# Kernel optimization log

Measured on AMD Instinct MI355X. Metric: run time of the kernel, lower is better.

The kernel has to match this reference:

```python
import jax, jax.numpy as jnp
import numpy as np
import math

B, T, C = 2, 2048, 1024
H, D = 16, 64
GAMMA = 8

def setup_inputs() -> dict:
    key = jax.random.key(0)
    ks = jax.random.split(key, 6)
    s = 1.0 / math.sqrt(C)  # keep pre-softmax scores well-scaled
    return {
        "x": jax.random.normal(ks[0], (B, T, C), jnp.float32),
        "Wq": jax.random.normal(ks[1], (C, 2 * C), jnp.float32) * s,
        "Wk": jax.random.normal(ks[2], (C, 2 * C), jnp.float32) * s,
        "Wv": jax.random.normal(ks[3], (C, C), jnp.float32) * s,
        "Wo": jax.random.normal(ks[4], (C, C), jnp.float32) * s,
        "theta_offset": jax.random.normal(ks[5], (H,), jnp.float32) * 0.1,
    }

def _heads(t):  # (B,T,C) -> (B,H,T,D)
    return t.reshape(B, T, H, D).transpose(0, 2, 1, 3)

def reference(x, Wq, Wk, Wv, Wo, theta_offset):
    scale = 1.0 / math.sqrt(D)
    q_raw = x @ Wq            # (B,T,2C)
    k_raw = x @ Wk
    v = _heads(x @ Wv)        # (B,H,T,D)
    q_amp, q_phase = _heads(q_raw[..., :C]), _heads(q_raw[..., C:])
    k_amp, k_phase = _heads(k_raw[..., :C]), _heads(k_raw[..., C:])
    q_amp = jax.nn.softplus(q_amp)
    k_amp = jax.nn.softplus(k_amp)
    # sum_d a_q a_k cos(p_q - p_k) = (a_q cos p_q)(a_k cos p_k) + (a_q sin p_q)(a_k sin p_k)
    qc, qs = q_amp * jnp.cos(q_phase), q_amp * jnp.sin(q_phase)
    kc, ks_ = k_amp * jnp.cos(k_phase), k_amp * jnp.sin(k_phase)
    scores = (jnp.einsum('bhqd,bhkd->bhqk', qc, kc)
              + jnp.einsum('bhqd,bhkd->bhqk', qs, ks_)) * scale
    if T > GAMMA:  # theta gating
        cid = jnp.arange(T, dtype=jnp.float32) / GAMMA
        cycle_dist = cid[None, :] - cid[:, None]          # (T,T): cid[j]-cid[i]
        gate = jnp.cos(theta_offset[:, None, None] * cycle_dist[None])  # (H,T,T)
        scores = scores * gate[None]
    causal = jnp.tril(jnp.ones((T, T), dtype=bool))
    scores = jnp.where(causal[None, None], scores, -jnp.inf)
    attn = jax.nn.softmax(scores, axis=-1)
    out = jnp.einsum('bhqk,bhkd->bhqd', attn, v)
    out = out.transpose(0, 2, 1, 3).reshape(B, T, C)
    return out @ Wo
```

## Files before the change

### kernel.cpp

```cpp
#include <hip/hip_runtime.h>
#include <cmath>

namespace {

constexpr int B_ = 2, T_ = 2048, C_ = 1024, H_ = 16;
constexpr float GAMMA_INV = 0.125f;
constexpr float SCALE = 0.125f;
constexpr float LOG2E = 1.4426950408889634f;
constexpr float THR2 = 11.5415603f;

typedef __attribute__((ext_vector_type(8))) short bf16x8;
typedef __attribute__((ext_vector_type(4))) float f32x4;
typedef unsigned short ushort_t;

__device__ __forceinline__ ushort_t f2bf(float x) {
  union { float f; unsigned int u; } v; v.f = x;
  unsigned int r = (v.u + 0x7fffu + ((v.u >> 16) & 1u)) >> 16;
  return (ushort_t)r;
}

__device__ __forceinline__ unsigned pk_bf16(float a, float b) {
  unsigned r;
  asm("v_cvt_pk_bf16_f32 %0, %1, %2" : "=v"(r) : "v"(a), "v"(b));
  return r;
}

__device__ __forceinline__ float fexp2(float x) {
  return __builtin_amdgcn_exp2f(x);
}

__device__ __forceinline__ f32x4 mfma16(bf16x8 a, bf16x8 b, f32x4 c) {
  return __builtin_amdgcn_mfma_f32_16x16x32_bf16(a, b, c, 0, 0, 0);
}

__device__ __forceinline__ void gld_lds16(const ushort_t* g, ushort_t* l) {
  __builtin_amdgcn_global_load_lds(
      (const __attribute__((address_space(1))) unsigned int*)g,
      (__attribute__((address_space(3))) unsigned int*)l, 16, 0, 0);
}

constexpr int GBM = 128, GBN = 128, GBK = 64;

#define GEMM_CORE(A_, Bt_, K_)                                                  \
  __shared__ ushort_t As[GBM][GBK];                                             \
  __shared__ ushort_t Bs[GBN][GBK];                                             \
  const int tid = threadIdx.x;                                                  \
  const int wv = tid >> 6;                                                      \
  const int ln = tid & 63;                                                      \
  const int lr = ln & 15, hi = ln >> 4;                                         \
  const int wr = wv >> 1, wc = wv & 1;                                          \
  const int srow8 = tid >> 3;                            \
  const int ssw = ((tid & 7) ^ (srow8 & 7)) * 8;       \
  const int kxg = (lr & 7) << 3;                    \
  f32x4 acc[4][4];                                                              \
  _Pragma("unroll")                                                             \
  for (int m = 0; m < 4; ++m)                                                   \
    _Pragma("unroll")                                                           \
    for (int n = 0; n < 4; ++n)                                                 \
      _Pragma("unroll")                                                         \
      for (int r = 0; r < 4; ++r) acc[m][n][r] = 0.0f;                          \
  for (int k0 = 0; k0 < K_; k0 += GBK) {                                        \
    _Pragma("unroll")                                                           \
    for (int p = 0; p < 4; ++p) {                                               \
      gld_lds16(A_ + (size_t)(m0 + p * 32 + srow8) * K_ + k0 + ssw,             \
                &As[0][0] + p * 2048 + wv * 512);                               \
      gld_lds16(Bt_ + (size_t)(n0 + p * 32 + srow8) * K_ + k0 + ssw,            \
                &Bs[0][0] + p * 2048 + wv * 512);                               \
    }                                                                           \
    __syncthreads();                                                            \
    _Pragma("unroll")                                                           \
    for (int ks = 0; ks < 2; ++ks) {                                            \
      bf16x8 af[4], bfr[4];                                                     \
      _Pragma("unroll")                                                         \
      for (int m = 0; m < 4; ++m)                                               \
        af[m] = *(const bf16x8*)&As[wr * 64 + m * 16 + lr]                      \
                                  [(ks * 32 + hi * 8) ^ kxg];                   \
      _Pragma("unroll")                                                         \
      for (int n = 0; n < 4; ++n)                                               \
        bfr[n] = *(const bf16x8*)&Bs[wc * 64 + n * 16 + lr]                     \
                                   [(ks * 32 + hi * 8) ^ kxg];                  \
      _Pragma("unroll")                                                         \
      for (int m = 0; m < 4; ++m)                                               \
        _Pragma("unroll")                                                       \
        for (int n = 0; n < 4; ++n)                                             \
          acc[m][n] = mfma16(af[m], bfr[n], acc[m][n]);                         \
    }                                                                           \
    __syncthreads();                                                            \
  }

__global__ __launch_bounds__(256) void gemm_f32out(const ushort_t* __restrict__ A,
                                                   const ushort_t* __restrict__ Bt,
                                                   float* __restrict__ Cm,
                                                   int N, int K) {
  const int m0 = blockIdx.y * GBM, n0 = blockIdx.x * GBN;
  GEMM_CORE(A, Bt, K)
  #pragma unroll
  for (int m = 0; m < 4; ++m) {
    #pragma unroll
    for (int r = 0; r < 4; ++r) {
      const int row = m0 + wr * 64 + m * 16 + hi * 4 + r;
      float* Crow = Cm + (size_t)row * N + n0 + wc * 64;
      #pragma unroll
      for (int n = 0; n < 4; ++n)
        Crow[n * 16 + lr] = acc[m][n][r];
    }
  }
}

__global__ __launch_bounds__(256) void gemm_qkv(const ushort_t* __restrict__ A,
                                                const ushort_t* __restrict__ Bt,
                                                ushort_t* __restrict__ Qb,
                                                ushort_t* __restrict__ Kb,
                                                float* __restrict__ Vf,
                                                int K) {
  const int m0 = blockIdx.y * GBM, n0 = blockIdx.x * GBN;
  GEMM_CORE(A, Bt, K)
  if (n0 < 4096) {
    const int isK = (n0 >> 11) & 1;
    ushort_t* Dst = isK ? Kb : Qb;
    const int odd = lr & 1;
    #pragma unroll
    for (int m = 0; m < 4; ++m) {
      #pragma unroll
      for (int r = 0; r < 4; ++r) {
        const int row = m0 + wr * 64 + m * 16 + hi * 4 + r;
        #pragma unroll
        for (int n = 0; n < 4; ++n) {
          const int nn = n0 + wc * 64 + n * 16 + lr;
          float x = acc[m][n][r];
          float y = __shfl_xor(x, 1);
          float amp = odd ? y : x;
          float ph  = odd ? x : y;
          float sp = (amp > 20.f) ? amp : __logf(1.0f + __expf(amp));
          float val = sp * (odd ? __sinf(ph) : __cosf(ph));
          const int cc = (nn & 2047) >> 1;
          const int h = cc >> 6, d = cc & 63;
          const int t = row & (T_ - 1), b = row >> 11;
          Dst[(((size_t)(b * H_ + h) * T_) + t) * 128 + d + (odd ? 64 : 0)] = f2bf(val);
        }
      }
    }
  } else {
    const int v0 = n0 - 4096;
    #pragma unroll
    for (int m = 0; m < 4; ++m) {
      #pragma unroll
      for (int r = 0; r < 4; ++r) {
        const int row = m0 + wr * 64 + m * 16 + hi * 4 + r;
        float* Crow = Vf + (size_t)row * 1024 + v0 + wc * 64;
        #pragma unroll
        for (int n = 0; n < 4; ++n)
          Crow[n * 16 + lr] = acc[m][n][r];
      }
    }
  }
}

__global__ __launch_bounds__(256) void f32_to_bf16(const float* __restrict__ in,
                                                   ushort_t* __restrict__ out) {
  const int i = (blockIdx.x * 256 + threadIdx.x) * 4;
  float4 a = *(const float4*)&in[i];
  uint2 p;
  p.x = (unsigned)f2bf(a.x) | ((unsigned)f2bf(a.y) << 16);
  p.y = (unsigned)f2bf(a.z) | ((unsigned)f2bf(a.w) << 16);
  *(uint2*)&out[i] = p;
}

__global__ __launch_bounds__(256) void wt_bf16(const float* __restrict__ W,
                                               ushort_t* __restrict__ Wt,
                                               int K, int N) {
  __shared__ ushort_t t[32][33];
  const int k0 = blockIdx.y * 32, n0 = blockIdx.x * 32;
  const int i = threadIdx.x;
  const int r = i >> 3, c4 = (i & 7) * 4;
  float4 v = *(const float4*)&W[(size_t)(k0 + r) * N + n0 + c4];
  t[r][c4 + 0] = f2bf(v.x); t[r][c4 + 1] = f2bf(v.y);
  t[r][c4 + 2] = f2bf(v.z); t[r][c4 + 3] = f2bf(v.w);
  __syncthreads();
  ushort_t o0 = t[c4 + 0][r], o1 = t[c4 + 1][r], o2 = t[c4 + 2][r], o3 = t[c4 + 3][r];
  uint2 p;
  p.x = (unsigned)o0 | ((unsigned)o1 << 16);
  p.y = (unsigned)o2 | ((unsigned)o3 << 16);
  *(uint2*)&Wt[(size_t)(n0 + r) * K + k0 + c4] = p;
}

__global__ __launch_bounds__(256) void wt_qk(const float* __restrict__ Wq,
                                             const float* __restrict__ Wk,
                                             ushort_t* __restrict__ Wqkt) {
  __shared__ float t[32][33];
  const int k0 = blockIdx.x * 32, n0 = blockIdx.y * 32;
  const float* src = (n0 < 2048) ? Wq : Wk;
  const int c0 = (n0 & 2047) >> 1;
  const int i = threadIdx.x;
  {
    const int r = i >> 3, c4 = (i & 7) * 4;
    const int scol = (c4 < 16) ? (c0 + c4) : (1024 + c0 + c4 - 16);
    float4 v = *(const float4*)&src[(size_t)(k0 + r) * 2048 + scol];
    t[r][c4 + 0] = v.x; t[r][c4 + 1] = v.y; t[r][c4 + 2] = v.z; t[r][c4 + 3] = v.w;
  }
  __syncthreads();
  {
    const int orow = i >> 3, k4 = (i & 7) * 4;
    const int sel = (orow >> 1) + ((orow & 1) ? 16 : 0);
    uint2 p;
    p.x = (unsigned)f2bf(t[k4 + 0][sel]) | ((unsigned)f2bf(t[k4 + 1][sel]) << 16);
    p.y = (unsigned)f2bf(t[k4 + 2][sel]) | ((unsigned)f2bf(t[k4 + 3][sel]) << 16);
    *(uint2*)&Wqkt[(size_t)(n0 + orow) * 1024 + k0 + k4] = p;
  }
}

__global__ __launch_bounds__(256) void v_transpose(const float* __restrict__ V,
                                                   ushort_t* __restrict__ VT) {
  const int bh = blockIdx.y;
  const int b = bh >> 4, h = bh & 15;
  const int t0 = blockIdx.x * 32;
  __shared__ ushort_t lds[32][72];
  const int i = threadIdx.x;
  {
    int r = i >> 3, d0 = (i & 7) * 8;
    const float* src = V + ((size_t)(b * T_) + t0 + r) * C_ + h * 64 + d0;
    float4 a = *(const float4*)src;
    float4 c = *(const float4*)(src + 4);
    lds[r][d0 + 0] = f2bf(a.x); lds[r][d0 + 1] = f2bf(a.y);
    lds[r][d0 + 2] = f2bf(a.z); lds[r][d0 + 3] = f2bf(a.w);
    lds[r][d0 + 4] = f2bf(c.x); lds[r][d0 + 5] = f2bf(c.y);
    lds[r][d0 + 6] = f2bf(c.z); lds[r][d0 + 7] = f2bf(c.w);
  }
  __syncthreads();
  {
    int d = i >> 2, tq = (i & 3) * 8;
    ushort_t tmp[8];
    #pragma unroll
    for (int j = 0; j < 8; ++j) tmp[j] = lds[tq + j][d];
    ulonglong2 pk;
    pk.x = (unsigned long long)tmp[0] | ((unsigned long long)tmp[1] << 16) |
           ((unsigned long long)tmp[2] << 32) | ((unsigned long long)tmp[3] << 48);
    pk.y = (unsigned long long)tmp[4] | ((unsigned long long)tmp[5] << 16) |
           ((unsigned long long)tmp[6] << 32) | ((unsigned long long)tmp[7] << 48);
    *(ulonglong2*)(VT + ((size_t)bh * 64 + d) * T_ + t0 + tq) = pk;
  }
}

__global__ __launch_bounds__(256) void attn_split(const ushort_t* __restrict__ Q,
                                                  const ushort_t* __restrict__ K,
                                                  const ushort_t* __restrict__ VT,
                                                  const float* __restrict__ theta,
                                                  unsigned* __restrict__ Op,
                                                  float* __restrict__ mpart,
                                                  float* __restrict__ lpart) {
  const int id = blockIdx.x;
  const int xcd = id & 7, sub = id >> 3;
  const int bhl = sub / 40;
  const int u = 39 - (sub - bhl * 40);
  int qt, s, ns;
  if (u < 4)       { qt = u;                 s = 0;             ns = 1; }
  else if (u < 12) { qt = 4 + ((u - 4) >> 1);  s = (u - 4) & 1;   ns = 2; }
  else if (u < 24) { qt = 8 + (u - 12) / 3;    s = (u - 12) % 3;  ns = 3; }
  else             { qt = 12 + ((u - 24) >> 2); s = (u - 24) & 3; ns = 4; }
  const int nktf = 2 * qt + 2;
  const int t0 = (s * nktf) / ns;
  const int t1 = ((s + 1) * nktf) / ns;
  const int bh = xcd * 4 + bhl;
  const int p = bh * 40 + u;
  unsigned* Op_my = Op + (size_t)p * 4096;

  const int h = bh & 15;
  const int tid = threadIdx.x;
  const int wid = tid >> 6, lane = tid & 63;
  const int q_base = qt * 128 + wid * 32;
  const int lr = lane & 15, lg = lane >> 4;
  const int kx = (lr & 7) << 4;

  __shared__ alignas(16) ushort_t Ksh[2][64 * 128];
  __shared__ alignas(16) ushort_t Vsh[64 * 64];

  const float th = theta[h];
  const int q_lo = q_base + lr;
  const int q_hi = q_base + 16 + lr;

  bf16x8 qfl[4], qfh[4];
  {
    const ushort_t* Qrow = Q + ((size_t)bh * T_ + q_lo) * 128 + lg * 8;
    #pragma unroll
    for (int ks = 0; ks < 4; ++ks) {
      qfl[ks] = *(const bf16x8*)(Qrow + ks * 32);
      qfh[ks] = *(const bf16x8*)(Qrow + 16 * 128 + ks * 32);
    }
  }

  const float cql = cosf(th * (float)q_lo * GAMMA_INV) * (SCALE * LOG2E);
  const float sql = sinf(th * (float)q_lo * GAMMA_INV) * (SCALE * LOG2E);
  const float cqh = cosf(th * (float)q_hi * GAMMA_INV) * (SCALE * LOG2E);
  const float sqh = sinf(th * (float)q_hi * GAMMA_INV) * (SCALE * LOG2E);
  float ck[4], sk[4];
  #pragma unroll
  for (int r = 0; r < 4; ++r) {
    float ang = th * (float)(t0 * 64 + lg * 4 + r) * GAMMA_INV;
    ck[r] = cosf(ang); sk[r] = sinf(ang);
  }
  float Ajl[4], Bjl[4], Ajh[4], Bjh[4];
  {
    const float c2 = cosf(th * 2.0f), s2 = sinf(th * 2.0f);
    float cj = 1.0f, sj = 0.0f;
    #pragma unroll
    for (int j = 0; j < 4; ++j) {
      Ajl[j] = cql * cj + sql * sj;
      Bjl[j] = sql * cj - cql * sj;
      Ajh[j] = cqh * cj + sqh * sj;
      Bjh[j] = sqh * cj - cqh * sj;
      float t0r = cj * c2 - sj * s2;
      sj = sj * c2 + cj * s2;
      cj = t0r;
    }
  }
  const float cd8 = cosf(th * 8.0f), sd8 = sinf(th * 8.0f);

  f32x4 o_lo[4], o_hi[4];
  #pragma unroll
  for (int n = 0; n < 4; ++n)
    #pragma unroll
    for (int r = 0; r < 4; ++r) { o_lo[n][r] = 0.0f; o_hi[n][r] = 0.0f; }
  float m_lo = -1e30f, l_lo = 0.0f, m_hi = -1e30f, l_hi = 0.0f;

  const ushort_t* Kbh = K + (size_t)bh * T_ * 128;
  const int srow = lane >> 4;
  const int scol = (lane & 15) * 8;
  const int vd = tid >> 2;
  const int vce = (tid & 3) * 16;
  const ushort_t* Vgb = VT + ((size_t)bh * 64 + vd) * T_ + vce;
  uint4 vreg[2];

  {
    const int k0 = t0 * 64;
    #pragma unroll
    for (int c = 0; c < 4; ++c) {
      const int r7 = 4 * (c & 1) + srow;
      const ushort_t* src = Kbh + (size_t)(k0 + 16 * wid + 4 * c + srow) * 128
                            + (scol ^ (r7 << 3));
      gld_lds16(src, &Ksh[0][(wid * 4 + c) * 512]);
    }
    #pragma unroll
    for (int c = 0; c < 2; ++c) vreg[c] = *(const uint4*)(Vgb + k0 + c * 8);
    #pragma unroll
    for (int c = 0; c < 2; ++c) {
      int byte = (vce * 2 + c * 16) ^ ((vd & 7) << 4);
      *(uint4*)&Vsh[vd * 64 + (byte >> 1)] = vreg[c];
    }
  }
  __syncthreads();

  for (int kt = t0; kt < t1; ++kt) {
    const int cur = (kt - t0) & 1;
    const int k0 = kt * 64;
    const bool more = (kt + 1) < t1;
    if (more) {
      const int kn = (kt + 1) * 64;
      #pragma unroll
      for (int c = 0; c < 4; ++c) {
        const int r7 = 4 * (c & 1) + srow;
        const ushort_t* src = Kbh + (size_t)(kn + 16 * wid + 4 * c + srow) * 128
                              + (scol ^ (r7 << 3));
        gld_lds16(src, &Ksh[cur ^ 1][(wid * 4 + c) * 512]);
      }
      #pragma unroll
      for (int c = 0; c < 2; ++c) vreg[c] = *(const uint4*)(Vgb + kn + c * 8);
    }
    f32x4 sl[4], sh[4];
    #pragma unroll
    for (int j = 0; j < 4; ++j)
      #pragma unroll
      for (int r = 0; r < 4; ++r) { sl[j][r] = 0.0f; sh[j][r] = 0.0f; }
    #pragma unroll
    for (int j = 0; j < 4; ++j) {
      const int rbase = (j * 16 + lr) * 128;
      #pragma unroll
      for (int ks = 0; ks < 4; ++ks) {
        const int byte = (ks * 64 + lg * 16) ^ kx;
        bf16x8 kf = *(const bf16x8*)&Ksh[cur][rbase + (byte >> 1)];
        sl[j] = mfma16(kf, qfl[ks], sl[j]);
        sh[j] = mfma16(kf, qfh[ks], sh[j]);
      }
    }
    float vl[4][4], vh[4][4];
    #pragma unroll
    for (int j = 0; j < 4; ++j)
      #pragma unroll
      for (int r = 0; r < 4; ++r) {
        const int kk = k0 + j * 16 + lg * 4 + r;
        float xl = sl[j][r] * (Ajl[j] * ck[r] + Bjl[j] * sk[r]);
        float xh = sh[j][r] * (Ajh[j] * ck[r] + Bjh[j] * sk[r]);
        vl[j][r] = (kk > q_lo) ? -3e30f : xl;
        vh[j][r] = (kk > q_hi) ? -3e30f : xh;
      }
    float tml = vl[0][0], tmh = vh[0][0];
    #pragma unroll
    for (int j = 0; j < 4; ++j)
      #pragma unroll
      for (int r = 0; r < 4; ++r) { tml = fmaxf(tml, vl[j][r]); tmh = fmaxf(tmh, vh[j][r]); }
    tml = fmaxf(tml, __shfl_xor(tml, 16));
    tml = fmaxf(tml, __shfl_xor(tml, 32));
    tmh = fmaxf(tmh, __shfl_xor(tmh, 16));
    tmh = fmaxf(tmh, __shfl_xor(tmh, 32));
    if (__ballot(tml > m_lo + THR2 || tmh > m_hi + THR2)) {
      float mnl = fmaxf(m_lo, tml), mnh = fmaxf(m_hi, tmh);
      float el = fexp2(m_lo - mnl), eh = fexp2(m_hi - mnh);
      m_lo = mnl; m_hi = mnh;
      l_lo *= el; l_hi *= eh;
      #pragma unroll
      for (int r = 0; r < 4; ++r) {
        float erl = __shfl(el, lg * 4 + r);
        float erh = __shfl(eh, lg * 4 + r);
        #pragma unroll
        for (int n = 0; n < 4; ++n) { o_lo[n][r] *= erl; o_hi[n][r] *= erh; }
      }
    }
    float el[4][4], eh[4][4], psl = 0.0f, psh = 0.0f;
    #pragma unroll
    for (int j = 0; j < 4; ++j)
      #pragma unroll
      for (int r = 0; r < 4; ++r) {
        el[j][r] = fexp2(vl[j][r] - m_lo);
        eh[j][r] = fexp2(vh[j][r] - m_hi);
        psl += el[j][r];
        psh += eh[j][r];
      }
    psl += __shfl_xor(psl, 16);
    psl += __shfl_xor(psl, 32);
    psh += __shfl_xor(psh, 16);
    psh += __shfl_xor(psh, 32);
    l_lo += psl; l_hi += psh;
    bf16x8 pal[2], pah[2];
    #pragma unroll
    for (int hh = 0; hh < 2; ++hh) {
      union { bf16x8 v8; unsigned u4[4]; } ul, uh;
      ul.u4[0] = pk_bf16(el[2 * hh][0], el[2 * hh][1]);
      ul.u4[1] = pk_bf16(el[2 * hh][2], el[2 * hh][3]);
      ul.u4[2] = pk_bf16(el[2 * hh + 1][0], el[2 * hh + 1][1]);
      ul.u4[3] = pk_bf16(el[2 * hh + 1][2], el[2 * hh + 1][3]);
      uh.u4[0] = pk_bf16(eh[2 * hh][0], eh[2 * hh][1]);
      uh.u4[1] = pk_bf16(eh[2 * hh][2], eh[2 * hh][3]);
      uh.u4[2] = pk_bf16(eh[2 * hh + 1][0], eh[2 * hh + 1][1]);
      uh.u4[3] = pk_bf16(eh[2 * hh + 1][2], eh[2 * hh + 1][3]);
      pal[hh] = ul.v8; pah[hh] = uh.v8;
    }
    #pragma unroll
    for (int n = 0; n < 4; ++n) {
      const int dbase = (n * 16 + lr) * 64;
      #pragma unroll
      for (int hh = 0; hh < 2; ++hh) {
        const int b0 = (hh * 64 + lg * 8) ^ kx;
        const int b1 = (hh * 64 + 32 + lg * 8) ^ kx;
        union { bf16x8 v8; uint2 u2[2]; } uu;
        uu.u2[0] = *(const uint2*)&Vsh[dbase + (b0 >> 1)];
        uu.u2[1] = *(const uint2*)&Vsh[dbase + (b1 >> 1)];
        o_lo[n] = mfma16(pal[hh], uu.v8, o_lo[n]);
        o_hi[n] = mfma16(pah[hh], uu.v8, o_hi[n]);
      }
    }
    #pragma unroll
    for (int r = 0; r < 4; ++r) {
      float t0r = ck[r] * cd8 - sk[r] * sd8;
      sk[r] = sk[r] * cd8 + ck[r] * sd8;
      ck[r] = t0r;
    }
    __syncthreads();
    if (more) {
      #pragma unroll
      for (int c = 0; c < 2; ++c) {
        int byte = (vce * 2 + c * 16) ^ ((vd & 7) << 4);
        *(uint4*)&Vsh[vd * 64 + (byte >> 1)] = vreg[c];
      }
      __syncthreads();
    }
  }
  #pragma unroll
  for (int r = 0; r < 4; ++r) {
    const int pr = wid * 16 + lg * 4 + r;
    #pragma unroll
    for (int n = 0; n < 4; ++n) {
      Op_my[pr * 64 + n * 16 + lr] =
          (unsigned)f2bf(o_lo[n][r]) | ((unsigned)f2bf(o_hi[n][r]) << 16);
    }
  }
  if (lg == 0) {
    mpart[p * 128 + wid * 32 + lr] = m_lo;
    lpart[p * 128 + wid * 32 + lr] = l_lo;
    mpart[p * 128 + wid * 32 + 16 + lr] = m_hi;
    lpart[p * 128 + wid * 32 + 16 + lr] = l_hi;
  }
}

__global__ __launch_bounds__(256) void attn_comb(const unsigned* __restrict__ Op,
                                                 const float* __restrict__ mpart,
                                                 const float* __restrict__ lpart,
                                                 ushort_t* __restrict__ O) {
  const int id = blockIdx.x;
  const int bh = id >> 4, qt = id & 15;
  const int b = bh >> 4, h = bh & 15;
  int base, ns;
  if (qt < 4)       { base = qt;                 ns = 1; }
  else if (qt < 8)  { base = 4 + 2 * (qt - 4);   ns = 2; }
  else if (qt < 12) { base = 12 + 3 * (qt - 8);  ns = 3; }
  else              { base = 24 + 4 * (qt - 12); ns = 4; }
  const int tid = threadIdx.x;
  const int r = tid >> 1, d0 = (tid & 1) * 32;
  const int pr = ((r >> 5) << 4) + (r & 15);
  const int hi = (r >> 4) & 1;

  float ms[4], ls[4];
  float M = -3e30f;
  for (int s2 = 0; s2 < ns; ++s2) {
    const int p = bh * 40 + base + s2;
    ms[s2] = mpart[p * 128 + r];
    ls[s2] = lpart[p * 128 + r];
    M = fmaxf(M, ms[s2]);
  }
  float acc[32];
  #pragma unroll
  for (int i = 0; i < 32; ++i) acc[i] = 0.0f;
  float denom = 0.0f;
  for (int s2 = 0; s2 < ns; ++s2) {
    const int p = bh * 40 + base + s2;
    const float w = fexp2(ms[s2] - M);
    denom += w * ls[s2];
    const unsigned* a = Op + (size_t)p * 4096 + pr * 64 + d0;
    #pragma unroll
    for (int c = 0; c < 8; ++c) {
      uint4 v = *(const uint4*)(a + c * 4);
      const unsigned uu[4] = {v.x, v.y, v.z, v.w};
      #pragma unroll
      for (int q2 = 0; q2 < 4; ++q2) {
        union { unsigned u; float f; } cv;
        cv.u = hi ? (uu[q2] & 0xFFFF0000u) : (uu[q2] << 16);
        acc[c * 4 + q2] += w * cv.f;
      }
    }
  }
  const float inv = 1.0f / denom;
  unsigned po[16];
  #pragma unroll
  for (int i = 0; i < 16; ++i)
    po[i] = (unsigned)f2bf(acc[2 * i] * inv) | ((unsigned)f2bf(acc[2 * i + 1] * inv) << 16);
  const int q = qt * 128 + r;
  ushort_t* dst = O + ((size_t)b * T_ + q) * C_ + h * 64 + d0;
  *(uint4*)(dst + 0)  = make_uint4(po[0], po[1], po[2], po[3]);
  *(uint4*)(dst + 8)  = make_uint4(po[4], po[5], po[6], po[7]);
  *(uint4*)(dst + 16) = make_uint4(po[8], po[9], po[10], po[11]);
  *(uint4*)(dst + 24) = make_uint4(po[12], po[13], po[14], po[15]);
}

}

extern "C" void kernel_launch(void* const* d_in, const int* in_sizes, int n_in,
                              void* d_out, int out_size, void* d_ws, size_t ws_size,
                              hipStream_t stream) {
  const float* x  = (const float*)d_in[0];
  const float* Wq = (const float*)d_in[1];
  const float* Wk = (const float*)d_in[2];
  const float* Wv = (const float*)d_in[3];
  const float* Wo = (const float*)d_in[4];
  const float* th = (const float*)d_in[5];
  float* out = (float*)d_out;
  float* ws = (float*)d_ws;

  unsigned* Op    = (unsigned*)ws;
  float* Vf       = ws;
  ushort_t* xb    = (ushort_t*)(ws + 4194304);
  ushort_t* Wqkvt = (ushort_t*)(ws + 6291456);
  ushort_t* Wvt   = Wqkvt + (size_t)4096 * 1024;
  ushort_t* Qb    = (ushort_t*)(ws + 10485760);
  ushort_t* Ob    = (ushort_t*)(ws + 10485760);
  ushort_t* Kb    = (ushort_t*)(ws + 14680064);
  ushort_t* vt    = (ushort_t*)(ws + 18874368);
  float* mpart    = ws + 20971520;
  float* lpart    = ws + 21135360;
  ushort_t* Wot   = (ushort_t*)(ws + 21495808);

  dim3 blk(256);
  f32_to_bf16<<<4096, blk, 0, stream>>>(x, xb);
  wt_qk<<<dim3(32, 128), blk, 0, stream>>>(Wq, Wk, Wqkvt);
  wt_bf16<<<dim3(32, 32), blk, 0, stream>>>(Wv, Wvt, 1024, 1024);
  wt_bf16<<<dim3(32, 32), blk, 0, stream>>>(Wo, Wot, 1024, 1024);
  gemm_qkv<<<dim3(40, 32), blk, 0, stream>>>(xb, Wqkvt, Qb, Kb, Vf, 1024);
  v_transpose<<<dim3(64, 32), blk, 0, stream>>>(Vf, vt);
  attn_split<<<1280, blk, 0, stream>>>(Qb, Kb, vt, th, Op, mpart, lpart);
  attn_comb<<<512, blk, 0, stream>>>(Op, mpart, lpart, Ob);
  gemm_f32out<<<dim3(8, 32), blk, 0, stream>>>(Ob, Wot, out, 1024, 1024);
}
```

Baseline: 206.2 us.

## Prefetch next GEMM K-tile into registers while computing current tile

```diff
diff --git a/kernel.cpp b/kernel.cpp
--- a/kernel.cpp
+++ b/kernel.cpp
@@ -50,8 +50,10 @@
   const int lr = ln & 15, hi = ln >> 4;                                         \
   const int wr = wv >> 1, wc = wv & 1;                                          \
   const int srow8 = tid >> 3;                            \
-  const int ssw = ((tid & 7) ^ (srow8 & 7)) * 8;       \
-  const int kxg = (lr & 7) << 3;                    \
+  const int ssw = ((tid & 7) ^ (srow8 & 7)) * 8;          \
+  const int sdc = (tid & 7) * 8;                       \
+  const int kxg = (lr & 7) << 3;                             \
+  uint4 ra[4], rb[4];                                                           \
   f32x4 acc[4][4];                                                              \
   _Pragma("unroll")                                                             \
   for (int m = 0; m < 4; ++m)                                                   \
@@ -59,15 +61,28 @@
     for (int n = 0; n < 4; ++n)                                                 \
       _Pragma("unroll")                                                         \
       for (int r = 0; r < 4; ++r) acc[m][n][r] = 0.0f;                          \
+  _Pragma("unroll")                                                             \
+  for (int p = 0; p < 4; ++p) {                                                 \
+    ra[p] = *(const uint4*)(A_ + (size_t)(m0 + p * 32 + srow8) * K_ + ssw);     \
+    rb[p] = *(const uint4*)(Bt_ + (size_t)(n0 + p * 32 + srow8) * K_ + ssw);    \
+  }                                                                             \
+  _Pragma("unroll")                                                             \
+  for (int p = 0; p < 4; ++p) {                                                 \
+    *(uint4*)&As[p * 32 + srow8][sdc] = ra[p];                                  \
+    *(uint4*)&Bs[p * 32 + srow8][sdc] = rb[p];                                  \
+  }                                                                             \
+  __syncthreads();                                                              \
   for (int k0 = 0; k0 < K_; k0 += GBK) {                                        \
-    _Pragma("unroll")                                                           \
-    for (int p = 0; p < 4; ++p) {                                               \
-      gld_lds16(A_ + (size_t)(m0 + p * 32 + srow8) * K_ + k0 + ssw,             \
-                &As[0][0] + p * 2048 + wv * 512);                               \
-      gld_lds16(Bt_ + (size_t)(n0 + p * 32 + srow8) * K_ + k0 + ssw,            \
-                &Bs[0][0] + p * 2048 + wv * 512);                               \
+    const bool more = (k0 + GBK) < K_;                                          \
+    if (more) {                                                                 \
+      _Pragma("unroll")                                                         \
+      for (int p = 0; p < 4; ++p) {                                             \
+        ra[p] = *(const uint4*)(A_ + (size_t)(m0 + p * 32 + srow8) * K_         \
+                                + k0 + GBK + ssw);                              \
+        rb[p] = *(const uint4*)(Bt_ + (size_t)(n0 + p * 32 + srow8) * K_        \
+                                + k0 + GBK + ssw);                              \
+      }                                                                         \
     }                                                                           \
-    __syncthreads();                                                            \
     _Pragma("unroll")                                                           \
     for (int ks = 0; ks < 2; ++ks) {                                            \
       bf16x8 af[4], bfr[4];                                                     \
@@ -86,6 +101,14 @@
           acc[m][n] = mfma16(af[m], bfr[n], acc[m][n]);                         \
     }                                                                           \
     __syncthreads();                                                            \
+    if (more) {                                                                 \
+      _Pragma("unroll")                                                         \
+      for (int p = 0; p < 4; ++p) {                                             \
+        *(uint4*)&As[p * 32 + srow8][sdc] = ra[p];                              \
+        *(uint4*)&Bs[p * 32 + srow8][sdc] = rb[p];                              \
+      }                                                                         \
+      __syncthreads();                                                          \
+    }                                                                           \
   }
 
 __global__ __launch_bounds__(256) void gemm_f32out(const ushort_t* __restrict__ A,
```

Measured after the change: 347.5 us. +68.5%, slower.
